# Kernel optimization log

Hardware: AMD Instinct MI355X
Metric: run time of the kernel (lower is better)

Reference implementation:

```python
import jax, jax.numpy as jnp
import numpy as np

CONFIGS = [(4, 2, 1, 1), (4, 4, 3, 3)]  # (k, stride, pad, dilation) per level


def conv2d(x, w, b, stride=1, pad=1):
    y = jax.lax.conv_general_dilated(x, w, (stride, stride), [(pad, pad), (pad, pad)],
                                     dimension_numbers=('NCHW', 'OIHW', 'NCHW'))
    return y + b[None, :, None, None]


def deform_conv(x, offset, mask, wgt, b, k, stride, pad, dil):
    """Modulated deformable conv v2 (zero padding, bilinear sampling).
    x: [B,Cin,Hin,Win]; offset: [B,2K,H,W] interleaved (dy_i,dx_i); mask: [B,K,H,W]."""
    B, Cin, Hin, Win = x.shape
    _, _, H, W = mask.shape
    K = k * k
    dy = offset[:, 0::2]  # [B,K,H,W]
    dx = offset[:, 1::2]
    ks = jnp.arange(k, dtype=offset.dtype) * dil
    kyf = jnp.repeat(ks, k)  # [K], ky-major to match weight.reshape(Cout,Cin,K)
    kxf = jnp.tile(ks, k)
    oy = jnp.arange(H, dtype=offset.dtype) * stride - pad
    ox = jnp.arange(W, dtype=offset.dtype) * stride - pad
    py = (kyf[:, None] + oy[None, :])[None, :, :, None] + dy  # [B,K,H,W]
    px = (kxf[:, None] + ox[None, :])[None, :, None, :] + dx

    def per_image(img, pyi, pxi, mi):
        imgf = img.reshape(Cin, -1)
        y0 = jnp.floor(pyi)
        x0 = jnp.floor(pxi)
        ly = pyi - y0
        lx = pxi - x0
        y0i = y0.astype(jnp.int32)
        x0i = x0.astype(jnp.int32)

        def corner(yi, xi, wt):
            valid = (yi >= 0) & (yi < Hin) & (xi >= 0) & (xi < Win)
            lin = (jnp.clip(yi, 0, Hin - 1) * Win + jnp.clip(xi, 0, Win - 1)).reshape(-1)
            v = imgf[:, lin].reshape(Cin, K, H, W)
            return v * (wt * valid)[None]

        s = (corner(y0i, x0i, (1 - ly) * (1 - lx))
             + corner(y0i, x0i + 1, (1 - ly) * lx)
             + corner(y0i + 1, x0i, ly * (1 - lx))
             + corner(y0i + 1, x0i + 1, ly * lx))
        return s * mi[None]  # [Cin,K,H,W]

    sampled = jax.vmap(per_image)(x, py, px, mask)  # [B,Cin,K,H,W]
    out = jnp.einsum('bikhw,oik->bohw', sampled, wgt.reshape(wgt.shape[0], Cin, K))
    return out + b[None, :, None, None]


def setup_inputs():
    key = jax.random.key(0)
    ks = jax.random.split(key, 16)
    B, C, H = 4, 256, 40
    K = 16  # k*k with k=4
    dcn_std = 1.0 / np.sqrt(C * K)
    res_std = 1.0 / np.sqrt(C * 9)
    return {
        'f0': jax.random.normal(ks[0], (B, C, H * 4, H * 4), jnp.float32),
        'f1': jax.random.normal(ks[1], (B, C, H * 2, H * 2), jnp.float32),
        'f2': jax.random.normal(ks[2], (B, C, H, H), jnp.float32),
        'com_w0': jax.random.normal(ks[3], (3 * K, C, 3, 3), jnp.float32) * 0.01,
        'com_b0': jax.random.normal(ks[4], (3 * K,), jnp.float32) * 0.01,
        'com_w1': jax.random.normal(ks[5], (3 * K, C, 3, 3), jnp.float32) * 0.01,
        'com_b1': jax.random.normal(ks[6], (3 * K,), jnp.float32) * 0.01,
        'dcn_w0': jax.random.normal(ks[7], (C, C, 4, 4), jnp.float32) * dcn_std,
        'dcn_b0': jnp.zeros((C,), jnp.float32),
        'dcn_w1': jax.random.normal(ks[8], (C, C, 4, 4), jnp.float32) * dcn_std,
        'dcn_b1': jnp.zeros((C,), jnp.float32),
        'res_w': jax.random.normal(ks[9], (C, C, 3, 3), jnp.float32) * res_std,
        'res_b': jnp.zeros((C,), jnp.float32),
    }


def reference(f0, f1, f2, com_w0, com_b0, com_w1, com_b1,
              dcn_w0, dcn_b0, dcn_w1, dcn_b1, res_w, res_b):
    features = [f0, f1, f2]
    com = [(com_w0, com_b0), (com_w1, com_b1)]
    dcn = [(dcn_w0, dcn_b0), (dcn_w1, dcn_b1)]
    repeat, levels = 2, 3
    fh = features[-1]
    f = fh
    for _ in range(repeat):
        for l in range(levels - 1):
            k, s, p, d = CONFIGS[l]
            K = k * k
            om = conv2d(f, com[l][0], com[l][1])
            offset = jnp.concatenate([om[:, :K], om[:, K:2 * K]], axis=1)
            m = jax.nn.sigmoid(om[:, 2 * K:])
            dc = deform_conv(features[levels - 2 - l], offset, m, dcn[l][0], dcn[l][1], k, s, p, d)
            f = jax.nn.relu(dc) + f
    return fh + conv2d(f, res_w, res_b)
```

## Files before the change

### kernel.cpp

```cpp
#include <hip/hip_runtime.h>

#define HW40 1600
typedef unsigned short ushort_t;
typedef __attribute__((ext_vector_type(8))) short short8;
typedef __attribute__((ext_vector_type(4))) short short4v;
typedef __attribute__((ext_vector_type(4))) float f4v;

__device__ __forceinline__ float bu(ushort_t u) {
  union { unsigned i; float f; } x; x.i = ((unsigned)u) << 16; return x.f;
}
__device__ __forceinline__ ushort_t fb(float f) {
  union { float f; unsigned i; } x; x.f = f;
  unsigned r = x.i + 0x7FFFu + ((x.i >> 16) & 1u);
  return (ushort_t)(r >> 16);
}

#define GLD16(g, l)                                                            \
  __builtin_amdgcn_global_load_lds(                                            \
      (const __attribute__((address_space(1))) void*)(g),                      \
      (__attribute__((address_space(3))) void*)(l), 16, 0, 0)

#define PART_STRIDE 1638400

__global__ void zp_init(ushort_t* zp) { zp[threadIdx.x] = 0; }

__global__ void convert_w9(const float* __restrict__ src, ushort_t* __restrict__ dst,
                           int Cout_src, int Cout_pad) {
  int idx = blockIdx.x * 256 + threadIdx.x;
  if (idx >= Cout_pad * 2304) return;
  int co = idx / 2304;
  int k  = idx - co * 2304;
  int cin = k & 255, tap = k >> 8;
  dst[idx] = (co < Cout_src) ? fb(src[(size_t)co * 2304 + cin * 9 + tap]) : (ushort_t)0;
}

__global__ __launch_bounds__(256) void convert_dcnw(const float* __restrict__ w0,
                                                    const float* __restrict__ w1,
                                                    ushort_t* __restrict__ A0,
                                                    ushort_t* __restrict__ A1) {
  __shared__ float s[4096];
  const int co = blockIdx.x & 255;
  const float* w = (blockIdx.x < 256) ? w0 : w1;
  ushort_t* A = (blockIdx.x < 256) ? A0 : A1;
  const int t = threadIdx.x;
  const float4* wp = (const float4*)(w + (size_t)co * 4096);
#pragma unroll
  for (int q = 0; q < 4; ++q) ((float4*)s)[t + q * 256] = wp[t + q * 256];
  __syncthreads();
  const int i = t >> 4, cb = (t & 15) * 16;
  ushort_t tmp[16];
#pragma unroll
  for (int j = 0; j < 16; ++j) tmp[j] = fb(s[(cb + j) * 16 + i]);
  ushort_t* op = A + (size_t)co * 4096 + t * 16;
  ((uint4*)op)[0] = ((uint4*)tmp)[0];
  ((uint4*)op)[1] = ((uint4*)tmp)[1];
}

__global__ __launch_bounds__(256) void nhwc_bf16_kernel(const float* __restrict__ x,
                                                        ushort_t* __restrict__ xt, int HW) {
  __shared__ float tile[32][33];
  const int s0 = blockIdx.x * 32, c0 = blockIdx.y * 32, b = blockIdx.z;
  const int tx = threadIdx.x & 31, ty = threadIdx.x >> 5;
  const float* xb = x + ((size_t)b * 256 + c0) * HW + s0;
#pragma unroll
  for (int q = 0; q < 4; ++q) tile[ty + q * 8][tx] = xb[(size_t)(ty + q * 8) * HW + tx];
  __syncthreads();
  ushort_t* ob = xt + ((size_t)b * HW + s0) * 256 + c0;
#pragma unroll
  for (int q = 0; q < 4; ++q) {
    int srow = ty + q * 8;
    ob[(size_t)srow * 256 + tx] = fb(tile[tx][srow]);
  }
}

__global__ __launch_bounds__(256) void sample_kernel(
    const ushort_t* __restrict__ xt, const ushort_t* __restrict__ part,
    const float* __restrict__ cbias, ushort_t* __restrict__ colT,
    int Hin, int Win, int stride, int pad, int dil) {
  __shared__ int4  gL[128];
  __shared__ float4 gW[128];
  const int g = blockIdx.x;
  const int work = (g & 7) * 100 + (g >> 3);
  const int b = work / 200;
  const int px0 = (work - b * 200) * 8;
  const int t = threadIdx.x;
  const int HWin = Hin * Win;

  if (t < 128) {
    const int px_l = t & 7, i = t >> 3;
    const int p = px0 + px_l;
    const int n = b * 1600 + p;
    const int ph = p / 40, pw = p - (p / 40) * 40;
    float dy = cbias[2 * i], dx = cbias[2 * i + 1], mzr = cbias[32 + i];
#pragma unroll
    for (int kz = 0; kz < 4; ++kz) {
      const ushort_t* pp = part + (size_t)kz * PART_STRIDE + n;
      dy  += bu(pp[(size_t)(2 * i) * 6400]);
      dx  += bu(pp[(size_t)(2 * i + 1) * 6400]);
      mzr += bu(pp[(size_t)(32 + i) * 6400]);
    }
    float mz = 1.f / (1.f + expf(-mzr));
    float py = (float)(ph * stride - pad + (i >> 2) * dil) + dy;
    float px = (float)(pw * stride - pad + (i & 3) * dil) + dx;
    float y0f = floorf(py), x0f = floorf(px);
    float ly = py - y0f, lx = px - x0f;
    int y0 = (int)y0f, x0 = (int)x0f;
    int y1 = y0 + 1, x1 = x0 + 1;
    float hy = 1.f - ly, hx = 1.f - lx;
    float w00 = hy * hx * mz, w01 = hy * lx * mz;
    float w10 = ly * hx * mz, w11 = ly * lx * mz;
    if (y0 < 0 || y0 >= Hin) { w00 = 0.f; w01 = 0.f; }
    if (y1 < 0 || y1 >= Hin) { w10 = 0.f; w11 = 0.f; }
    if (x0 < 0 || x0 >= Win) { w00 = 0.f; w10 = 0.f; }
    if (x1 < 0 || x1 >= Win) { w01 = 0.f; w11 = 0.f; }
    int cy0 = min(max(y0, 0), Hin - 1), cy1 = min(max(y1, 0), Hin - 1);
    int cx0 = min(max(x0, 0), Win - 1), cx1 = min(max(x1, 0), Win - 1);
    gL[t] = make_int4((cy0 * Win + cx0) * 256, (cy0 * Win + cx1) * 256,
                      (cy1 * Win + cx0) * 256, (cy1 * Win + cx1) * 256);
    gW[t] = make_float4(w00, w01, w10, w11);
  }
  __syncthreads();

  const ushort_t* xtb = xt + (size_t)b * HWin * 256;
  const int wv = t >> 6, l = t & 63;
  const int half = l >> 5;
  const int cin8 = (l & 31) * 8;

#pragma unroll 2
  for (int it = 0; it < 16; ++it) {
    const int pr = it * 8 + wv * 2 + half;
    const int4 G = gL[pr];
    const float4 W = gW[pr];
    short8 c00 = *(const short8*)(xtb + G.x + cin8);
    short8 c01 = *(const short8*)(xtb + G.y + cin8);
    short8 c10 = *(const short8*)(xtb + G.z + cin8);
    short8 c11 = *(const short8*)(xtb + G.w + cin8);
    short8 rr;
#pragma unroll
    for (int j = 0; j < 8; ++j) {
      float v = W.x * bu((ushort_t)c00[j]) + W.y * bu((ushort_t)c01[j]) +
                W.z * bu((ushort_t)c10[j]) + W.w * bu((ushort_t)c11[j]);
      rr[j] = (short)fb(v);
    }
    const int px_l = pr & 7, i = pr >> 3;
    *(short8*)(colT + ((size_t)(b * 1600 + px0 + px_l) * 4096 + i * 256 + cin8)) = rr;
  }
}

__global__ __launch_bounds__(256) void gemm_deform(const ushort_t* __restrict__ A,
                                                   const ushort_t* __restrict__ B,
                                                   ushort_t* __restrict__ part) {
  __shared__ ushort_t sA[128 * 32];
  __shared__ ushort_t sB[128 * 32];
  const int g = blockIdx.x;
  const int kz = g & 7, mt = (g >> 3) & 1, nt = g >> 4;
  const int t = threadIdx.x;
  const int wv = t >> 6, l = t & 63;
  const int wm = wv >> 1, wn = wv & 1;

  f4v acc[4][4];
#pragma unroll
  for (int a = 0; a < 4; ++a)
#pragma unroll
    for (int bb = 0; bb < 4; ++bb) acc[a][bb] = (f4v)(0.f);

  const int ra = t >> 2;
  const int q  = ((t & 3) - (ra >> 1)) & 3;
  const size_t aoff = (size_t)(mt * 128 + ra) * 4096 + q * 8;
  const size_t boff = (size_t)(nt * 128 + ra) * 4096 + q * 8;
  ushort_t* lA = sA + t * 8;
  ushort_t* lB = sB + t * 8;

  int k0 = kz * 512;
  const int lm = l & 15;
  const int koff = (((l >> 4) + (lm >> 1)) & 3) * 8;

  for (int step = 0; step < 16; ++step, k0 += 32) {
    __syncthreads();
    GLD16(A + aoff + k0, lA);
    GLD16(A + aoff + (size_t)64 * 4096 + k0, lA + 2048);
    GLD16(B + boff + k0, lB);
    GLD16(B + boff + (size_t)64 * 4096 + k0, lB + 2048);
    __syncthreads();
    short8 af[4], bfr[4];
#pragma unroll
    for (int fm = 0; fm < 4; ++fm)
      af[fm] = *(const short8*)(sA + (wm * 64 + fm * 16 + lm) * 32 + koff);
#pragma unroll
    for (int fn = 0; fn < 4; ++fn)
      bfr[fn] = *(const short8*)(sB + (wn * 64 + fn * 16 + lm) * 32 + koff);
#pragma unroll
    for (int fm = 0; fm < 4; ++fm)
#pragma unroll
      for (int fn = 0; fn < 4; ++fn)
        acc[fm][fn] = __builtin_amdgcn_mfma_f32_16x16x32_bf16(af[fm], bfr[fn],
                                                              acc[fm][fn], 0, 0, 0);
  }

  const int row_l = (l >> 4) * 4;
  ushort_t* pb = part + (size_t)kz * PART_STRIDE;
#pragma unroll
  for (int fm = 0; fm < 4; ++fm) {
#pragma unroll
    for (int fn = 0; fn < 4; ++fn) {
      const int n = nt * 128 + wn * 64 + fn * 16 + lm;
#pragma unroll
      for (int r = 0; r < 4; ++r) {
        const int m = mt * 128 + wm * 64 + fm * 16 + row_l + r;
        pb[(size_t)m * 6400 + n] = fb(acc[fm][fn][r]);
      }
    }
  }
}

template <int MTILE, int KZ>
__global__ __launch_bounds__(256) void gemm_conv3(const ushort_t* __restrict__ A,
                                                  const ushort_t* __restrict__ ft,
                                                  const ushort_t* __restrict__ zp,
                                                  ushort_t* __restrict__ part,
                                                  int ksteps) {
  constexpr int FN = (MTILE == 128) ? 4 : 2;
  __shared__ ushort_t sA[MTILE * 32];
  __shared__ ushort_t sB[128 * 32];
  const int g = blockIdx.x;
  const int kz = g % KZ;
  const int r = g / KZ;
  const int mt = (MTILE == 128) ? (r & 1) : 0;
  const int nt = (MTILE == 128) ? (r >> 1) : r;
  const int t = threadIdx.x;
  const int wv = t >> 6, l = t & 63;
  const int wm = (MTILE == 128) ? (wv >> 1) : 0;
  const int wn = (MTILE == 128) ? (wv & 1) : wv;

  f4v acc[4][FN];
#pragma unroll
  for (int a = 0; a < 4; ++a)
#pragma unroll
    for (int bb = 0; bb < FN; ++bb) acc[a][bb] = (f4v)(0.f);

  const int ra = t >> 2;
  const int q  = ((t & 3) - (ra >> 1)) & 3;
  const int qc = q * 8;
  const size_t aoff = (size_t)(mt * MTILE + ra) * 2304 + qc;
  const int n0 = nt * 128 + ra;
  const int n1 = n0 + 64;
  const int b0 = n0 / 1600, p0 = n0 - b0 * 1600;
  const int b1 = n1 / 1600, p1 = n1 - b1 * 1600;
  const int ph0 = p0 / 40, pw0 = p0 - (p0 / 40) * 40;
  const int ph1 = p1 / 40, pw1 = p1 - (p1 / 40) * 40;
  const ushort_t* fp0 = ft + (size_t)n0 * 256 + qc;
  const ushort_t* fp1 = ft + (size_t)n1 * 256 + qc;
  ushort_t* lA = sA + t * 8;
  ushort_t* lB = sB + t * 8;

  int k0 = kz * ksteps * 32;
  const int lm = l & 15;
  const int koff = (((l >> 4) + (lm >> 1)) & 3) * 8;

  for (int step = 0; step < ksteps; ++step, k0 += 32) {
    const int tap = k0 >> 8, c0 = k0 & 255;
    const int ky = tap / 3;
    const int dy = ky - 1, dx = (tap - ky * 3) - 1;
    const int off = (dy * 40 + dx) * 256 + c0;
    const bool ok0 = ((unsigned)(ph0 + dy) < 40u) & ((unsigned)(pw0 + dx) < 40u);
    const bool ok1 = ((unsigned)(ph1 + dy) < 40u) & ((unsigned)(pw1 + dx) < 40u);
    const ushort_t* s0 = ok0 ? (fp0 + off) : zp;
    const ushort_t* s1 = ok1 ? (fp1 + off) : zp;
    __syncthreads();
    GLD16(A + aoff + k0, lA);
    if (MTILE == 128) GLD16(A + aoff + (size_t)64 * 2304 + k0, lA + 2048);
    GLD16(s0, lB);
    GLD16(s1, lB + 2048);
    __syncthreads();
    short8 af[4], bfr[FN];
#pragma unroll
    for (int fm = 0; fm < 4; ++fm)
      af[fm] = *(const short8*)(sA + (wm * 64 + fm * 16 + lm) * 32 + koff);
#pragma unroll
    for (int fn = 0; fn < FN; ++fn)
      bfr[fn] = *(const short8*)(sB + (wn * (16 * FN) + fn * 16 + lm) * 32 + koff);
#pragma unroll
    for (int fm = 0; fm < 4; ++fm)
#pragma unroll
      for (int fn = 0; fn < FN; ++fn)
        acc[fm][fn] = __builtin_amdgcn_mfma_f32_16x16x32_bf16(af[fm], bfr[fn],
                                                              acc[fm][fn], 0, 0, 0);
  }

  const int row_l = (l >> 4) * 4;
  ushort_t* pb = part + (size_t)kz * PART_STRIDE;
#pragma unroll
  for (int fm = 0; fm < 4; ++fm) {
#pragma unroll
    for (int fn = 0; fn < FN; ++fn) {
      const int n = nt * 128 + wn * (16 * FN) + fn * 16 + lm;
#pragma unroll
      for (int r = 0; r < 4; ++r) {
        const int m = mt * MTILE + wm * 64 + fm * 16 + row_l + r;
        pb[(size_t)m * 6400 + n] = fb(acc[fm][fn][r]);
      }
    }
  }
}

__global__ __launch_bounds__(256) void gemm_epilogue(const ushort_t* __restrict__ part,
                                                     const float* __restrict__ bias,
                                                     const float* __restrict__ src,
                                                     float* __restrict__ dst, int relu) {
  const int co = blockIdx.y, b = blockIdx.z;
  const int idx = blockIdx.x * 256 + threadIdx.x;
  if (idx >= 400) return;
  const int p = idx * 4;
  const size_t n = (size_t)b * 1600 + p;
  float a[4] = {0.f, 0.f, 0.f, 0.f};
#pragma unroll
  for (int kz = 0; kz < 8; ++kz) {
    short4v pp = *(const short4v*)(part + (size_t)kz * PART_STRIDE + (size_t)co * 6400 + n);
#pragma unroll
    for (int j = 0; j < 4; ++j) a[j] += bu((ushort_t)pp[j]);
  }
  float bv = bias[co];
  const size_t fo = ((size_t)b * 256 + co) * 1600 + p;
  float4 s = *(const float4*)(src + fo);
  float4 o;
  if (relu) {
    o.x = fmaxf(a[0] + bv, 0.f) + s.x;
    o.y = fmaxf(a[1] + bv, 0.f) + s.y;
    o.z = fmaxf(a[2] + bv, 0.f) + s.z;
    o.w = fmaxf(a[3] + bv, 0.f) + s.w;
  } else {
    o.x = a[0] + bv + s.x;
    o.y = a[1] + bv + s.y;
    o.z = a[2] + bv + s.z;
    o.w = a[3] + bv + s.w;
  }
  *(float4*)(dst + fo) = o;
}

extern "C" void kernel_launch(void* const* d_in, const int* in_sizes, int n_in,
                              void* d_out, int out_size, void* d_ws, size_t ws_size,
                              hipStream_t stream) {
  (void)in_sizes; (void)n_in; (void)out_size; (void)ws_size;
  const float* f0     = (const float*)d_in[0];
  const float* f1     = (const float*)d_in[1];
  const float* f2     = (const float*)d_in[2];
  const float* com_w0 = (const float*)d_in[3];
  const float* com_b0 = (const float*)d_in[4];
  const float* com_w1 = (const float*)d_in[5];
  const float* com_b1 = (const float*)d_in[6];
  const float* dcn_w0 = (const float*)d_in[7];
  const float* dcn_b0 = (const float*)d_in[8];
  const float* dcn_w1 = (const float*)d_in[9];
  const float* dcn_b1 = (const float*)d_in[10];
  const float* res_w  = (const float*)d_in[11];
  const float* res_b  = (const float*)d_in[12];
  float* out = (float*)d_out;
  float* ws  = (float*)d_ws;

  float*    fbuf  = ws + 0;
  ushort_t* A0    = (ushort_t*)(ws + 1700000);
  ushort_t* A1    = (ushort_t*)(ws + 2230000);
  ushort_t* Acom0 = (ushort_t*)(ws + 2760000);
  ushort_t* Acom1 = (ushort_t*)(ws + 2840000);
  ushort_t* Ares  = (ushort_t*)(ws + 2920000);
  ushort_t* ft40  = (ushort_t*)(ws + 3220000);
  ushort_t* f1t   = (ushort_t*)(ws + 4050000);
  ushort_t* f0t   = (ushort_t*)(ws + 7330000);
  ushort_t* colT  = (ushort_t*)(ws + 20440000);
  ushort_t* part  = (ushort_t*)(ws + 33550000);
  ushort_t* zp    = (ushort_t*)(ws + 40110000);

  zp_init<<<1, 256, 0, stream>>>(zp);
  convert_w9<<<(64 * 2304 + 255) / 256, 256, 0, stream>>>(com_w0, Acom0, 48, 64);
  convert_w9<<<(64 * 2304 + 255) / 256, 256, 0, stream>>>(com_w1, Acom1, 48, 64);
  convert_w9<<<(256 * 2304 + 255) / 256, 256, 0, stream>>>(res_w, Ares, 256, 256);
  convert_dcnw<<<512, 256, 0, stream>>>(dcn_w0, dcn_w1, A0, A1);
  nhwc_bf16_kernel<<<dim3(200, 8, 4), 256, 0, stream>>>(f1, f1t, 6400);
  nhwc_bf16_kernel<<<dim3(800, 8, 4), 256, 0, stream>>>(f0, f0t, 25600);

  const float* fsrc = f2;
  for (int s = 0; s < 4; ++s) {
    int l = s & 1;
    nhwc_bf16_kernel<<<dim3(50, 8, 4), 256, 0, stream>>>(fsrc, ft40, 1600);
    gemm_conv3<64, 4><<<200, 256, 0, stream>>>(l ? Acom1 : Acom0, ft40, zp, part, 18);
    if (l == 0) {
      sample_kernel<<<800, 256, 0, stream>>>(f1t, part, com_b0, colT, 80, 80, 2, 1, 1);
    } else {
      sample_kernel<<<800, 256, 0, stream>>>(f0t, part, com_b1, colT, 160, 160, 4, 3, 3);
    }
    gemm_deform<<<800, 256, 0, stream>>>(l ? A1 : A0, colT, part);
    gemm_epilogue<<<dim3(2, 256, 4), 256, 0, stream>>>(part, l ? dcn_b1 : dcn_b0, fsrc, fbuf, 1);
    fsrc = fbuf;
  }
  nhwc_bf16_kernel<<<dim3(50, 8, 4), 256, 0, stream>>>(fbuf, ft40, 1600);
  gemm_conv3<128, 8><<<800, 256, 0, stream>>>(Ares, ft40, zp, part, 9);
  gemm_epilogue<<<dim3(2, 256, 4), 256, 0, stream>>>(part, res_b, f2, out, 0);
}
```

Measured before the change: 567.8 us.

## Fuse prep kernels, fold NHWC conversion into epilogue, resplit com conv

```diff
diff --git a/kernel.cpp b/kernel.cpp
--- a/kernel.cpp
+++ b/kernel.cpp
@@ -22,44 +22,60 @@
 
 #define PART_STRIDE 1638400
 
-__global__ void zp_init(ushort_t* zp) { zp[threadIdx.x] = 0; }
-
-__global__ void convert_w9(const float* __restrict__ src, ushort_t* __restrict__ dst,
-                           int Cout_src, int Cout_pad) {
-  int idx = blockIdx.x * 256 + threadIdx.x;
-  if (idx >= Cout_pad * 2304) return;
-  int co = idx / 2304;
-  int k  = idx - co * 2304;
-  int cin = k & 255, tap = k >> 8;
-  dst[idx] = (co < Cout_src) ? fb(src[(size_t)co * 2304 + cin * 9 + tap]) : (ushort_t)0;
-}
-
-__global__ __launch_bounds__(256) void convert_dcnw(const float* __restrict__ w0,
-                                                    const float* __restrict__ w1,
-                                                    ushort_t* __restrict__ A0,
-                                                    ushort_t* __restrict__ A1) {
+__global__ __launch_bounds__(256) void prep_all(
+    const float* __restrict__ com_w0, const float* __restrict__ com_w1,
+    const float* __restrict__ res_w, const float* __restrict__ dcn_w0,
+    const float* __restrict__ dcn_w1, ushort_t* __restrict__ Acom0,
+    ushort_t* __restrict__ Acom1, ushort_t* __restrict__ Ares,
+    ushort_t* __restrict__ A0, ushort_t* __restrict__ A1,
+    ushort_t* __restrict__ zp) {
   __shared__ float s[4096];
-  const int co = blockIdx.x & 255;
-  const float* w = (blockIdx.x < 256) ? w0 : w1;
-  ushort_t* A = (blockIdx.x < 256) ? A0 : A1;
+  const int g = blockIdx.x;
   const int t = threadIdx.x;
-  const float4* wp = (const float4*)(w + (size_t)co * 4096);
-#pragma unroll
-  for (int q = 0; q < 4; ++q) ((float4*)s)[t + q * 256] = wp[t + q * 256];
-  __syncthreads();
-  const int i = t >> 4, cb = (t & 15) * 16;
-  ushort_t tmp[16];
-#pragma unroll
-  for (int j = 0; j < 16; ++j) tmp[j] = fb(s[(cb + j) * 16 + i]);
-  ushort_t* op = A + (size_t)co * 4096 + t * 16;
-  ((uint4*)op)[0] = ((uint4*)tmp)[0];
-  ((uint4*)op)[1] = ((uint4*)tmp)[1];
-}
-
-__global__ __launch_bounds__(256) void nhwc_bf16_kernel(const float* __restrict__ x,
-                                                        ushort_t* __restrict__ xt, int HW) {
+  if (g < 3456) {
+    const float* src; ushort_t* dst; int Cout_src; int base;
+    if (g < 576)       { src = com_w0; dst = Acom0; Cout_src = 48;  base = g; }
+    else if (g < 1152) { src = com_w1; dst = Acom1; Cout_src = 48;  base = g - 576; }
+    else               { src = res_w;  dst = Ares;  Cout_src = 256; base = g - 1152; }
+    const int idx = base * 256 + t;
+    const int co = idx / 2304;
+    const int k  = idx - co * 2304;
+    const int cin = k & 255, tap = k >> 8;
+    dst[idx] = (co < Cout_src) ? fb(src[(size_t)co * 2304 + cin * 9 + tap]) : (ushort_t)0;
+  } else if (g < 3968) {
+    const int lg = g - 3456;
+    const int co = lg & 255;
+    const float* w = (lg < 256) ? dcn_w0 : dcn_w1;
+    ushort_t* A = (lg < 256) ? A0 : A1;
+    const float4* wp = (const float4*)(w + (size_t)co * 4096);
+#pragma unroll
+    for (int q = 0; q < 4; ++q) ((float4*)s)[t + q * 256] = wp[t + q * 256];
+    __syncthreads();
+    const int i = t >> 4, cb = (t & 15) * 16;
+    ushort_t tmp[16];
+#pragma unroll
+    for (int j = 0; j < 16; ++j) tmp[j] = fb(s[(cb + j) * 16 + i]);
+    ushort_t* op = A + (size_t)co * 4096 + t * 16;
+    ((uint4*)op)[0] = ((uint4*)tmp)[0];
+    ((uint4*)op)[1] = ((uint4*)tmp)[1];
+  } else {
+    zp[t] = 0;
+  }
+}
+
+__global__ __launch_bounds__(256) void nhwc_all(const float* __restrict__ f2,
+                                                const float* __restrict__ f1,
+                                                const float* __restrict__ f0,
+                                                ushort_t* __restrict__ ft40,
+                                                ushort_t* __restrict__ f1t,
+                                                ushort_t* __restrict__ f0t) {
   __shared__ float tile[32][33];
-  const int s0 = blockIdx.x * 32, c0 = blockIdx.y * 32, b = blockIdx.z;
+  const int gx = blockIdx.x;
+  const float* x; ushort_t* xt; int HW, sblk;
+  if (gx < 50)       { x = f2; xt = ft40; HW = 1600;  sblk = gx; }
+  else if (gx < 250) { x = f1; xt = f1t;  HW = 6400;  sblk = gx - 50; }
+  else               { x = f0; xt = f0t;  HW = 25600; sblk = gx - 250; }
+  const int s0 = sblk * 32, c0 = blockIdx.y * 32, b = blockIdx.z;
   const int tx = threadIdx.x & 31, ty = threadIdx.x >> 5;
   const float* xb = x + ((size_t)b * 256 + c0) * HW + s0;
 #pragma unroll
@@ -93,7 +109,7 @@
     const int ph = p / 40, pw = p - (p / 40) * 40;
     float dy = cbias[2 * i], dx = cbias[2 * i + 1], mzr = cbias[32 + i];
 #pragma unroll
-    for (int kz = 0; kz < 4; ++kz) {
+    for (int kz = 0; kz < 8; ++kz) {
       const ushort_t* pp = part + (size_t)kz * PART_STRIDE + n;
       dy  += bu(pp[(size_t)(2 * i) * 6400]);
       dx  += bu(pp[(size_t)(2 * i + 1) * 6400]);
@@ -303,38 +319,54 @@
   }
 }
 
-__global__ __launch_bounds__(256) void gemm_epilogue(const ushort_t* __restrict__ part,
-                                                     const float* __restrict__ bias,
-                                                     const float* __restrict__ src,
-                                                     float* __restrict__ dst, int relu) {
-  const int co = blockIdx.y, b = blockIdx.z;
-  const int idx = blockIdx.x * 256 + threadIdx.x;
-  if (idx >= 400) return;
-  const int p = idx * 4;
-  const size_t n = (size_t)b * 1600 + p;
-  float a[4] = {0.f, 0.f, 0.f, 0.f};
+__global__ __launch_bounds__(256) void epi_fused(const ushort_t* __restrict__ part,
+                                                 const float* __restrict__ bias,
+                                                 const float* __restrict__ src,
+                                                 float* __restrict__ dst,
+                                                 ushort_t* __restrict__ ft, int relu) {
+  __shared__ __align__(16) ushort_t tile[32][72];
+  const int t = threadIdx.x;
+  const int p0 = blockIdx.x * 64, c0 = blockIdx.y * 32, b = blockIdx.z;
+  const int co_l = t >> 3, pg = t & 7;
+  const int co = c0 + co_l;
+  const size_t n = (size_t)b * 1600 + p0 + pg * 8;
+
+  float a[8] = {0.f, 0.f, 0.f, 0.f, 0.f, 0.f, 0.f, 0.f};
 #pragma unroll
   for (int kz = 0; kz < 8; ++kz) {
-    short4v pp = *(const short4v*)(part + (size_t)kz * PART_STRIDE + (size_t)co * 6400 + n);
-#pragma unroll
-    for (int j = 0; j < 4; ++j) a[j] += bu((ushort_t)pp[j]);
-  }
-  float bv = bias[co];
-  const size_t fo = ((size_t)b * 256 + co) * 1600 + p;
-  float4 s = *(const float4*)(src + fo);
-  float4 o;
-  if (relu) {
-    o.x = fmaxf(a[0] + bv, 0.f) + s.x;
-    o.y = fmaxf(a[1] + bv, 0.f) + s.y;
-    o.z = fmaxf(a[2] + bv, 0.f) + s.z;
-    o.w = fmaxf(a[3] + bv, 0.f) + s.w;
-  } else {
-    o.x = a[0] + bv + s.x;
-    o.y = a[1] + bv + s.y;
-    o.z = a[2] + bv + s.z;
-    o.w = a[3] + bv + s.w;
-  }
-  *(float4*)(dst + fo) = o;
+    short8 pp = *(const short8*)(part + (size_t)kz * PART_STRIDE + (size_t)co * 6400 + n);
+#pragma unroll
+    for (int j = 0; j < 8; ++j) a[j] += bu((ushort_t)pp[j]);
+  }
+  const float bv = bias[co];
+  const size_t fo = ((size_t)b * 256 + co) * 1600 + p0 + pg * 8;
+  float4 s0 = *(const float4*)(src + fo);
+  float4 s1 = *(const float4*)(src + fo + 4);
+  const float sv[8] = {s0.x, s0.y, s0.z, s0.w, s1.x, s1.y, s1.z, s1.w};
+  float o[8];
+#pragma unroll
+  for (int j = 0; j < 8; ++j) {
+    float v = a[j] + bv;
+    if (relu) v = fmaxf(v, 0.f);
+    o[j] = v + sv[j];
+  }
+  float4 o0 = {o[0], o[1], o[2], o[3]};
+  float4 o1 = {o[4], o[5], o[6], o[7]};
+  *(float4*)(dst + fo) = o0;
+  *(float4*)(dst + fo + 4) = o1;
+
+  if (ft) {
+    short8 rr;
+#pragma unroll
+    for (int j = 0; j < 8; ++j) rr[j] = (short)fb(o[j]);
+    *(short8*)(&tile[co_l][pg * 8]) = rr;
+    __syncthreads();
+    const int p_l = t >> 2, cb = (t & 3) * 8;
+    short8 v;
+#pragma unroll
+    for (int j = 0; j < 8; ++j) v[j] = (short)tile[cb + j][p_l];
+    *(short8*)(ft + ((size_t)(b * 1600 + p0 + p_l)) * 256 + c0 + cb) = v;
+  }
 }
 
 extern "C" void kernel_launch(void* const* d_in, const int* in_sizes, int n_in,
@@ -370,29 +402,24 @@
   ushort_t* part  = (ushort_t*)(ws + 33550000);
   ushort_t* zp    = (ushort_t*)(ws + 40110000);
 
-  zp_init<<<1, 256, 0, stream>>>(zp);
-  convert_w9<<<(64 * 2304 + 255) / 256, 256, 0, stream>>>(com_w0, Acom0, 48, 64);
-  convert_w9<<<(64 * 2304 + 255) / 256, 256, 0, stream>>>(com_w1, Acom1, 48, 64);
-  convert_w9<<<(256 * 2304 + 255) / 256, 256, 0, stream>>>(res_w, Ares, 256, 256);
-  convert_dcnw<<<512, 256, 0, stream>>>(dcn_w0, dcn_w1, A0, A1);
-  nhwc_bf16_kernel<<<dim3(200, 8, 4), 256, 0, stream>>>(f1, f1t, 6400);
-  nhwc_bf16_kernel<<<dim3(800, 8, 4), 256, 0, stream>>>(f0, f0t, 25600);
+  prep_all<<<3969, 256, 0, stream>>>(com_w0, com_w1, res_w, dcn_w0, dcn_w1,
+                                     Acom0, Acom1, Ares, A0, A1, zp);
+  nhwc_all<<<dim3(1050, 8, 4), 256, 0, stream>>>(f2, f1, f0, ft40, f1t, f0t);
 
   const float* fsrc = f2;
   for (int s = 0; s < 4; ++s) {
     int l = s & 1;
-    nhwc_bf16_kernel<<<dim3(50, 8, 4), 256, 0, stream>>>(fsrc, ft40, 1600);
-    gemm_conv3<64, 4><<<200, 256, 0, stream>>>(l ? Acom1 : Acom0, ft40, zp, part, 18);
+    gemm_conv3<64, 8><<<400, 256, 0, stream>>>(l ? Acom1 : Acom0, ft40, zp, part, 9);
     if (l == 0) {
       sample_kernel<<<800, 256, 0, stream>>>(f1t, part, com_b0, colT, 80, 80, 2, 1, 1);
     } else {
       sample_kernel<<<800, 256, 0, stream>>>(f0t, part, com_b1, colT, 160, 160, 4, 3, 3);
     }
     gemm_deform<<<800, 256, 0, stream>>>(l ? A1 : A0, colT, part);
-    gemm_epilogue<<<dim3(2, 256, 4), 256, 0, stream>>>(part, l ? dcn_b1 : dcn_b0, fsrc, fbuf, 1);
+    epi_fused<<<dim3(25, 8, 4), 256, 0, stream>>>(part, l ? dcn_b1 : dcn_b0, fsrc,
+                                                  fbuf, ft40, 1);
     fsrc = fbuf;
   }
-  nhwc_bf16_kernel<<<dim3(50, 8, 4), 256, 0, stream>>>(fbuf, ft40, 1600);
   gemm_conv3<128, 8><<<800, 256, 0, stream>>>(Ares, ft40, zp, part, 9);
-  gemm_epilogue<<<dim3(2, 256, 4), 256, 0, stream>>>(part, res_b, f2, out, 0);
-}
+  epi_fused<<<dim3(25, 8, 4), 256, 0, stream>>>(part, res_b, f2, out, nullptr, 0);
+}
```

Measured after the change: 558.8 us. About the same (-1.6%).
